# Performance work log

Hardware: AMD Instinct MI355X
Metric: run time of the kernel (lower is better)

Reference implementation:

```python
import jax, jax.numpy as jnp
import numpy as np

EMBED_DIM = 64
HEAD_NUM = 16
BS, QL, KL = 4, 2048, 2048


def setup_inputs() -> dict:
    key = jax.random.key(0)
    k1, k2, k3, k4, k5, k6, k7, k8 = jax.random.split(key, 8)
    d, H = EMBED_DIM, HEAD_NUM
    q_origin = jax.random.normal(k1, (BS, QL, d), dtype=jnp.float32)
    k_origin = jax.random.normal(k2, (BS, KL, d), dtype=jnp.float32)
    mask = jax.random.randint(k3, (BS, QL, KL), 0, 2).astype(bool)
    scale = 1.0 / np.sqrt(d)
    Wq = jax.random.normal(k4, (d, d * H), dtype=jnp.float32) * scale
    Wk = jax.random.normal(k5, (d, d * H), dtype=jnp.float32) * scale
    Wv = jax.random.normal(k6, (d, d * H), dtype=jnp.float32) * scale
    Wfc = jax.random.normal(k7, (d, d), dtype=jnp.float32) * scale
    bfc = jax.random.normal(k8, (d,), dtype=jnp.float32) * 0.01
    return {"q_origin": q_origin, "k_origin": k_origin, "mask": mask,
            "Wq": Wq, "Wk": Wk, "Wv": Wv, "Wfc": Wfc, "bfc": bfc}


def reference(q_origin, k_origin, mask, Wq, Wk, Wv, Wfc, bfc):
    bs, ql, d = q_origin.shape
    _, kl, _ = k_origin.shape
    H = Wq.shape[1] // d
    # projections, split into H heads of width d
    q = (q_origin @ Wq).reshape(bs, ql, H, d)   # bqhd
    k = (k_origin @ Wk).reshape(bs, kl, H, d)   # bkhd
    v = (k_origin @ Wv).reshape(bs, kl, H, d)   # bkhd
    scores = jnp.einsum('bqhd,bkhd->bhqk', q, k)
    scores = jnp.where(mask[:, None, :, :], -jnp.inf, scores)
    attn = jax.nn.softmax(scores / jnp.sqrt(jnp.asarray(d, scores.dtype)), axis=-1)
    attn = jnp.nan_to_num(attn)
    out = jnp.einsum('bhqk,bkhd->bqhd', attn, v)
    # torch code concatenates heads along the sequence axis: (bs, ql*H, d)
    out = out.reshape(bs, ql * H, d)
    return jnp.tanh(out @ Wfc + bfc)
```

## Files before the change

kernel.cpp:

```cpp
#include <hip/hip_runtime.h>
#include <hip/hip_bf16.h>

#define BSZ 4
#define SEQ 2048
#define NH  16
#define DH  64
#define TOK (BSZ*SEQ)
#define PROJC (NH*DH)

typedef __bf16 bf16x8 __attribute__((ext_vector_type(8)));
typedef float  f32x4  __attribute__((ext_vector_type(4)));
typedef float  f32x16 __attribute__((ext_vector_type(16)));
typedef unsigned int uint4v __attribute__((ext_vector_type(4)));
typedef unsigned int uint2v __attribute__((ext_vector_type(2)));

__device__ inline unsigned short f2bf(float f) {
    __bf16 h = (__bf16)f;
    return __builtin_bit_cast(unsigned short, h);
}

__device__ inline bf16x8 ld8(const unsigned short* p) {
    return __builtin_bit_cast(bf16x8, *reinterpret_cast<const uint4v*>(p));
}

__device__ inline float fexp2(float x) {
    float r;
    asm("v_exp_f32 %0, %1" : "=v"(r) : "v"(x));
    return r;
}

__device__ inline void gload16(const unsigned short* g, unsigned short* l) {
    __builtin_amdgcn_global_load_lds(
        (__attribute__((address_space(1))) void*)g,
        (__attribute__((address_space(3))) void*)l, 16, 0, 0);
}

__global__ __launch_bounds__(256) void prep_kernel(const float* __restrict__ q,
                                                   const float* __restrict__ k,
                                                   const float* __restrict__ Wq,
                                                   const float* __restrict__ Wk,
                                                   const float* __restrict__ Wv,
                                                   const float* __restrict__ Wfc,
                                                   unsigned short* __restrict__ qbf,
                                                   unsigned short* __restrict__ kbf,
                                                   unsigned short* __restrict__ WqT,
                                                   unsigned short* __restrict__ WkT,
                                                   unsigned short* __restrict__ WvT,
                                                   unsigned short* __restrict__ WfcT) {
    int bx = blockIdx.x;
    if (bx < 4096) {
        int idx = (bx & 2047) * 256 + threadIdx.x;
        if (bx < 2048) qbf[idx] = f2bf(q[idx]);
        else           kbf[idx] = f2bf(k[idx]);
        return;
    }
    bx -= 4096;
    const float* W; unsigned short* WT; int cols; int base;
    if      (bx < 256) { W = Wq;  WT = WqT;  cols = PROJC; base = bx; }
    else if (bx < 512) { W = Wk;  WT = WkT;  cols = PROJC; base = bx - 256; }
    else if (bx < 768) { W = Wv;  WT = WvT;  cols = PROJC; base = bx - 512; }
    else               { W = Wfc; WT = WfcT; cols = 64;    base = bx - 768; }
    int idx = base * 256 + threadIdx.x;
    int c = idx % cols, kk = idx / cols;
    WT[c * 64 + kk] = f2bf(W[kk * cols + c]);
}

__global__ __launch_bounds__(256) void maskpack_kernel(const int* __restrict__ mask,
                                                       unsigned long long* __restrict__ mbits) {
    size_t gid = (size_t)blockIdx.x * 256 + threadIdx.x;
    int lane = threadIdx.x & 63;
    unsigned long long bal = __ballot(mask[gid] != 0);
    if (lane == 0) mbits[gid >> 6] = bal;
}

__global__ __launch_bounds__(256) void proj_kernel(const unsigned short* __restrict__ qbf,
                                                   const unsigned short* __restrict__ kbf,
                                                   const unsigned short* __restrict__ WqT,
                                                   const unsigned short* __restrict__ WkT,
                                                   const unsigned short* __restrict__ WvT,
                                                   unsigned short* __restrict__ Qo,
                                                   unsigned short* __restrict__ Ko,
                                                   unsigned short* __restrict__ Vto) {
    __shared__ __align__(16) unsigned short TQ[64][72];
    __shared__ __align__(16) unsigned short TK[64][72];
    __shared__ __align__(16) unsigned short TV[64][72];
    int tid = threadIdx.x, w = tid >> 6, lane = tid & 63;
    int l15 = lane & 15, l4 = lane >> 4;
    int r0 = blockIdx.x * 64 + w * 16;
    int h = blockIdx.y;
    int c0 = h * 64;
    int b = blockIdx.x >> 5;
    size_t bh = (size_t)(b * NH + h);

    const unsigned short* aq = qbf + (r0 + l15) * 64 + l4 * 8;
    bf16x8 a0q = ld8(aq), a1q = ld8(aq + 32);
    const unsigned short* ak = kbf + (r0 + l15) * 64 + l4 * 8;
    bf16x8 a0k = ld8(ak), a1k = ld8(ak + 32);

    #pragma unroll
    for (int ct = 0; ct < 4; ++ct) {
        int wrow = (c0 + ct * 16 + l15) * 64 + l4 * 8;
        bf16x8 q0 = ld8(WqT + wrow), q1 = ld8(WqT + wrow + 32);
        bf16x8 k0 = ld8(WkT + wrow), k1 = ld8(WkT + wrow + 32);
        bf16x8 v0 = ld8(WvT + wrow), v1 = ld8(WvT + wrow + 32);
        f32x4 accq = {0.f,0.f,0.f,0.f}, acck = accq, accv = accq;
        accq = __builtin_amdgcn_mfma_f32_16x16x32_bf16(q0, a0q, accq, 0, 0, 0);
        accq = __builtin_amdgcn_mfma_f32_16x16x32_bf16(q1, a1q, accq, 0, 0, 0);
        acck = __builtin_amdgcn_mfma_f32_16x16x32_bf16(k0, a0k, acck, 0, 0, 0);
        acck = __builtin_amdgcn_mfma_f32_16x16x32_bf16(k1, a1k, acck, 0, 0, 0);
        accv = __builtin_amdgcn_mfma_f32_16x16x32_bf16(a0k, v0, accv, 0, 0, 0);
        accv = __builtin_amdgcn_mfma_f32_16x16x32_bf16(a1k, v1, accv, 0, 0, 0);
        uint2v pq, pk, pv;
        pq.x = (unsigned)f2bf(accq[0]) | ((unsigned)f2bf(accq[1]) << 16);
        pq.y = (unsigned)f2bf(accq[2]) | ((unsigned)f2bf(accq[3]) << 16);
        pk.x = (unsigned)f2bf(acck[0]) | ((unsigned)f2bf(acck[1]) << 16);
        pk.y = (unsigned)f2bf(acck[2]) | ((unsigned)f2bf(acck[3]) << 16);
        pv.x = (unsigned)f2bf(accv[0]) | ((unsigned)f2bf(accv[1]) << 16);
        pv.y = (unsigned)f2bf(accv[2]) | ((unsigned)f2bf(accv[3]) << 16);
        *reinterpret_cast<uint2v*>(&TQ[w * 16 + l15][ct * 16 + l4 * 4]) = pq;
        *reinterpret_cast<uint2v*>(&TK[w * 16 + l15][ct * 16 + l4 * 4]) = pk;
        *reinterpret_cast<uint2v*>(&TV[ct * 16 + l15][w * 16 + l4 * 4]) = pv;
    }
    __syncthreads();

    int rl8 = tid >> 3, chunk = tid & 7;
    int q0 = (blockIdx.x & 31) * 64;
    #pragma unroll
    for (int p = 0; p < 2; ++p) {
        int rl = p * 32 + rl8;
        uint4v vq = *reinterpret_cast<const uint4v*>(&TQ[rl][chunk * 8]);
        uint4v vk = *reinterpret_cast<const uint4v*>(&TK[rl][chunk * 8]);
        uint4v vv = *reinterpret_cast<const uint4v*>(&TV[rl][chunk * 8]);
        *reinterpret_cast<uint4v*>(Qo  + (bh * SEQ + q0 + rl) * 64 + chunk * 8) = vq;
        *reinterpret_cast<uint4v*>(Ko  + (bh * SEQ + q0 + rl) * 64 + chunk * 8) = vk;
        *reinterpret_cast<uint4v*>(Vto + (bh * 64 + rl) * SEQ + q0 + chunk * 8) = vv;
    }
}

__global__ __launch_bounds__(512, 4) void attn_kernel(const unsigned short* __restrict__ Q,
                                                      const unsigned short* __restrict__ K,
                                                      const unsigned short* __restrict__ Vt,
                                                      const unsigned long long* __restrict__ mbits,
                                                      unsigned short* __restrict__ O) {
    __shared__ __align__(16) unsigned short Ks[2][64 * 64];
    __shared__ __align__(16) unsigned short Vs[2][64 * 64];
    int tid = threadIdx.x, w = tid >> 6, lane = tid & 63;
    int l31 = lane & 31, hi = lane >> 5;
    int hi4 = hi * 4;

    int bid = blockIdx.x;
    int swz = (bid & 7) * 64 + (bid >> 3);
    int bh = swz >> 3;
    int qt = swz & 7;
    int b = bh >> 4;
    int qbase = qt * 256 + w * 32;

    const unsigned short* Qh = Q  + (size_t)bh * SEQ * 64;
    const unsigned short* Kh = K  + (size_t)bh * SEQ * 64;
    const unsigned short* Vh = Vt + (size_t)bh * 64 * SEQ;
    const unsigned long long* mrow =
        mbits + ((size_t)b * SEQ + qbase + l31) * (SEQ / 64);

    int row1 = (w << 3) + (lane >> 3);
    int sc1 = (lane & 7) ^ (row1 & 7);
    unsigned short* Kd0 = &Ks[0][0] + w * 512;
    unsigned short* Vd0 = &Vs[0][0] + w * 512;
    unsigned short* Kd1 = &Ks[1][0] + w * 512;
    unsigned short* Vd1 = &Vs[1][0] + w * 512;

    bf16x8 qf[4];
    #pragma unroll
    for (int s = 0; s < 4; ++s)
        qf[s] = ld8(Qh + (size_t)(qbase + l31) * 64 + s * 16 + hi * 8);

    bf16x8 ones;
    #pragma unroll
    for (int i = 0; i < 8; ++i) ones[i] = (__bf16)1.0f;

    f32x16 o0 = {0.f,0.f,0.f,0.f,0.f,0.f,0.f,0.f,0.f,0.f,0.f,0.f,0.f,0.f,0.f,0.f};
    f32x16 o1 = o0;
    f32x16 ellD = o0;
    const float C = 0.125f * 1.44269504088896f;

    auto stage_tile = [&](unsigned short* Kd, unsigned short* Vd, int nkb) {
        gload16(Kh + (size_t)(nkb + row1) * 64 + sc1 * 8, Kd);
        gload16(Vh + (size_t)row1 * SEQ + nkb + sc1 * 8, Vd);
    };

    auto compute_tile = [&](const unsigned short* Kc, const unsigned short* Vc, int kb) {
        unsigned long long wb = mrow[kb >> 6];
        #pragma unroll
        for (int kt = 0; kt < 2; ++kt) {
            f32x16 z = {0.f,0.f,0.f,0.f,0.f,0.f,0.f,0.f,0.f,0.f,0.f,0.f,0.f,0.f,0.f,0.f};
            int krow = kt * 32 + l31;
            #pragma unroll
            for (int s = 0; s < 4; ++s) {
                const unsigned short* kp =
                    Kc + krow * 64 + ((((s << 1) + hi) ^ (krow & 7)) << 3);
                z = __builtin_amdgcn_mfma_f32_32x32x16_bf16(ld8(kp), qf[s], z, 0, 0, 0);
            }
            unsigned wsh = (unsigned)(wb >> (kt * 32)) >> hi4;
            unsigned wpk[8];
            #pragma unroll
            for (int rq = 0; rq < 4; ++rq) {
                #pragma unroll
                for (int rr = 0; rr < 2; ++rr) {
                    float e[2];
                    #pragma unroll
                    for (int j = 0; j < 2; ++j) {
                        int pos = rq * 8 + 2 * rr + j;
                        int sx = (int)(wsh << (31 - pos)) >> 31;
                        float bias = __builtin_bit_cast(float, (unsigned)sx & 0xFF800000u);
                        e[j] = fexp2(__builtin_fmaf(z[rq * 4 + 2 * rr + j], C, bias));
                    }
                    wpk[rq * 2 + rr] = (unsigned)f2bf(e[0]) | ((unsigned)f2bf(e[1]) << 16);
                }
            }
            __builtin_amdgcn_s_setprio(1);
            #pragma unroll
            for (int sl = 0; sl < 2; ++sl) {
                uint4v aw = {wpk[sl * 4 + 0], wpk[sl * 4 + 1],
                             wpk[sl * 4 + 2], wpk[sl * 4 + 3]};
                bf16x8 af = __builtin_bit_cast(bf16x8, aw);
                ellD = __builtin_amdgcn_mfma_f32_32x32x16_bf16(af, ones, ellD, 0, 0, 0);
                int n = kt * 2 + sl;
                {
                    int vrow = l31;
                    int c0i = ((2 * n) ^ (vrow & 7)) << 3;
                    int c1i = ((2 * n + 1) ^ (vrow & 7)) << 3;
                    uint2v lo = *reinterpret_cast<const uint2v*>(Vc + vrow * 64 + c0i + hi4);
                    uint2v hh = *reinterpret_cast<const uint2v*>(Vc + vrow * 64 + c1i + hi4);
                    uint4v vw = {lo.x, lo.y, hh.x, hh.y};
                    o0 = __builtin_amdgcn_mfma_f32_32x32x16_bf16(
                        af, __builtin_bit_cast(bf16x8, vw), o0, 0, 0, 0);
                }
                {
                    int vrow = 32 + l31;
                    int c0i = ((2 * n) ^ (vrow & 7)) << 3;
                    int c1i = ((2 * n + 1) ^ (vrow & 7)) << 3;
                    uint2v lo = *reinterpret_cast<const uint2v*>(Vc + vrow * 64 + c0i + hi4);
                    uint2v hh = *reinterpret_cast<const uint2v*>(Vc + vrow * 64 + c1i + hi4);
                    uint4v vw = {lo.x, lo.y, hh.x, hh.y};
                    o1 = __builtin_amdgcn_mfma_f32_32x32x16_bf16(
                        af, __builtin_bit_cast(bf16x8, vw), o1, 0, 0, 0);
                }
            }
            __builtin_amdgcn_s_setprio(0);
        }
    };

    stage_tile(Kd0, Vd0, 0);
    __syncthreads();

    for (int kb = 0; kb < SEQ; kb += 128) {
        stage_tile(Kd1, Vd1, kb + 64);
        compute_tile(&Ks[0][0], &Vs[0][0], kb);
        __syncthreads();
        if (kb + 128 < SEQ) stage_tile(Kd0, Vd0, kb + 128);
        compute_tile(&Ks[1][0], &Vs[1][0], kb + 64);
        __syncthreads();
    }
    #pragma unroll
    for (int reg = 0; reg < 16; ++reg) {
        float l = ellD[reg];
        float rcp = (l == 0.f) ? 0.f : __builtin_amdgcn_rcpf(l);
        int ql = (reg & 3) + 8 * (reg >> 2) + hi4;
        size_t base = ((size_t)bh * SEQ + qbase + ql) * 64 + l31;
        O[base]      = f2bf(o0[reg] * rcp);
        O[base + 32] = f2bf(o1[reg] * rcp);
    }
}

__global__ __launch_bounds__(256) void fc_kernel(const unsigned short* __restrict__ O,
                                                 const unsigned short* __restrict__ WfcT,
                                                 const float* __restrict__ bfc,
                                                 float* __restrict__ out) {
    int tid = threadIdx.x, w = tid >> 6, lane = tid & 63;
    int l15 = lane & 15, l4 = lane >> 4;
    int r0 = blockIdx.x * 64 + w * 16;

    int row = r0 + l15;
    int h = row & 15, t_ = row >> 4;
    int q = t_ & 2047, b = t_ >> 11;
    const unsigned short* op = O + (((size_t)(b * NH + h)) * SEQ + q) * 64 + l4 * 8;
    bf16x8 a0 = ld8(op), a1 = ld8(op + 32);

    for (int ct = 0; ct < 4; ++ct) {
        const unsigned short* wp = WfcT + (ct * 16 + l15) * 64 + l4 * 8;
        bf16x8 b0 = ld8(wp), b1 = ld8(wp + 32);
        f32x4 acc = {0.f, 0.f, 0.f, 0.f};
        acc = __builtin_amdgcn_mfma_f32_16x16x32_bf16(b0, a0, acc, 0, 0, 0);
        acc = __builtin_amdgcn_mfma_f32_16x16x32_bf16(b1, a1, acc, 0, 0, 0);
        f32x4 bv = *reinterpret_cast<const f32x4*>(bfc + ct * 16 + l4 * 4);
        f32x4 st;
        #pragma unroll
        for (int r = 0; r < 4; ++r) {
            float x = acc[r] + bv[r];
            x = fminf(fmaxf(x, -9.f), 9.f);
            float t = fexp2(x * 2.88539008177793f);
            st[r] = (t - 1.f) * __builtin_amdgcn_rcpf(t + 1.f);
        }
        *reinterpret_cast<f32x4*>(out + (size_t)row * 64 + ct * 16 + l4 * 4) = st;
    }
}

extern "C" void kernel_launch(void* const* d_in, const int* in_sizes, int n_in,
                              void* d_out, int out_size, void* d_ws, size_t ws_size,
                              hipStream_t stream) {
    const float* q_origin = (const float*)d_in[0];
    const float* k_origin = (const float*)d_in[1];
    const int*   mask     = (const int*)d_in[2];
    const float* Wq       = (const float*)d_in[3];
    const float* Wk       = (const float*)d_in[4];
    const float* Wv       = (const float*)d_in[5];
    const float* Wfc      = (const float*)d_in[6];
    const float* bfc      = (const float*)d_in[7];
    float* out = (float*)d_out;

    unsigned short* ws = (unsigned short*)d_ws;
    unsigned short* qbf  = ws;
    unsigned short* kbf  = qbf  + TOK * DH;
    unsigned short* WqT  = kbf  + TOK * DH;
    unsigned short* WkT  = WqT  + 64 * PROJC;
    unsigned short* WvT  = WkT  + 64 * PROJC;
    unsigned short* WfcT = WvT  + 64 * PROJC;
    unsigned short* Qb   = WfcT + 64 * 64;
    unsigned short* Kb   = Qb   + (size_t)BSZ * NH * SEQ * DH;
    unsigned short* Vtb  = Kb   + (size_t)BSZ * NH * SEQ * DH;
    unsigned short* Ob   = Vtb  + (size_t)BSZ * NH * SEQ * DH;
    unsigned long long* mbits = (unsigned long long*)d_ws;

    prep_kernel<<<4880, 256, 0, stream>>>(q_origin, k_origin, Wq, Wk, Wv, Wfc,
                                          qbf, kbf, WqT, WkT, WvT, WfcT);
    proj_kernel<<<dim3(TOK / 64, NH), 256, 0, stream>>>(
        qbf, kbf, WqT, WkT, WvT, Qb, Kb, Vtb);
    maskpack_kernel<<<(size_t)BSZ * SEQ * SEQ / 256, 256, 0, stream>>>(mask, mbits);
    attn_kernel<<<512, 512, 0, stream>>>(Qb, Kb, Vtb, mbits, Ob);
    fc_kernel<<<(size_t)BSZ * SEQ * NH / 64, 256, 0, stream>>>(Ob, WfcT, bfc, out);
}
```

Before: 175.0 us.

## Fuse output FC projection and tanh into attention kernel epilogue

The attention kernel now stages its normalized per-wave output tile into the freed K/V shared memory with an XOR swizzle. It then runs the 64x64 FC projection with 32x32x16 MFMAs, adds the bias and applies tanh before writing fp32 results directly. This removes the separate fc_kernel launch and the bf16 O round-trip through global memory. In exchange the attention epilogue gets longer and needs more registers, and WfcT is reloaded from global by every wave.

```diff
diff --git a/kernel.cpp b/kernel.cpp
--- a/kernel.cpp
+++ b/kernel.cpp
@@ -141,7 +141,9 @@
                                                       const unsigned short* __restrict__ K,
                                                       const unsigned short* __restrict__ Vt,
                                                       const unsigned long long* __restrict__ mbits,
-                                                      unsigned short* __restrict__ O) {
+                                                      const unsigned short* __restrict__ WfcT,
+                                                      const float* __restrict__ bfc,
+                                                      float* __restrict__ out) {
     __shared__ __align__(16) unsigned short Ks[2][64 * 64];
     __shared__ __align__(16) unsigned short Vs[2][64 * 64];
     int tid = threadIdx.x, w = tid >> 6, lane = tid & 63;
@@ -260,47 +262,49 @@
         compute_tile(&Ks[1][0], &Vs[1][0], kb + 64);
         __syncthreads();
     }
+
+    unsigned short* Ot = ((w < 4) ? &Ks[0][0] : &Vs[0][0]) + (w & 3) * 2048;
+
     #pragma unroll
     for (int reg = 0; reg < 16; ++reg) {
         float l = ellD[reg];
         float rcp = (l == 0.f) ? 0.f : __builtin_amdgcn_rcpf(l);
         int ql = (reg & 3) + 8 * (reg >> 2) + hi4;
-        size_t base = ((size_t)bh * SEQ + qbase + ql) * 64 + l31;
-        O[base]      = f2bf(o0[reg] * rcp);
-        O[base + 32] = f2bf(o1[reg] * rcp);
-    }
-}
-
-__global__ __launch_bounds__(256) void fc_kernel(const unsigned short* __restrict__ O,
-                                                 const unsigned short* __restrict__ WfcT,
-                                                 const float* __restrict__ bfc,
-                                                 float* __restrict__ out) {
-    int tid = threadIdx.x, w = tid >> 6, lane = tid & 63;
-    int l15 = lane & 15, l4 = lane >> 4;
-    int r0 = blockIdx.x * 64 + w * 16;
-
-    int row = r0 + l15;
-    int h = row & 15, t_ = row >> 4;
-    int q = t_ & 2047, b = t_ >> 11;
-    const unsigned short* op = O + (((size_t)(b * NH + h)) * SEQ + q) * 64 + l4 * 8;
-    bf16x8 a0 = ld8(op), a1 = ld8(op + 32);
-
-    for (int ct = 0; ct < 4; ++ct) {
-        const unsigned short* wp = WfcT + (ct * 16 + l15) * 64 + l4 * 8;
-        bf16x8 b0 = ld8(wp), b1 = ld8(wp + 32);
-        f32x4 acc = {0.f, 0.f, 0.f, 0.f};
-        acc = __builtin_amdgcn_mfma_f32_16x16x32_bf16(b0, a0, acc, 0, 0, 0);
-        acc = __builtin_amdgcn_mfma_f32_16x16x32_bf16(b1, a1, acc, 0, 0, 0);
-        f32x4 bv = *reinterpret_cast<const f32x4*>(bfc + ct * 16 + l4 * 4);
-        f32x4 st;
+        int ch0 = (l31 >> 3) ^ (ql & 7);
+        int ch1 = ((l31 >> 3) + 4) ^ (ql & 7);
+        Ot[ql * 64 + ch0 * 8 + (l31 & 7)] = f2bf(o0[reg] * rcp);
+        Ot[ql * 64 + ch1 * 8 + (l31 & 7)] = f2bf(o1[reg] * rcp);
+    }
+    bf16x8 of[4];
+    #pragma unroll
+    for (int s = 0; s < 4; ++s) {
+        int cs = (s * 2 + hi) ^ (l31 & 7);
+        of[s] = ld8(Ot + l31 * 64 + cs * 8);
+    }
+    int qrow = qbase + l31;
+    size_t orow = ((size_t)b * SEQ + qrow) * NH + (bh & 15);
+    #pragma unroll
+    for (int ctile = 0; ctile < 2; ++ctile) {
+        f32x16 acc = {0.f,0.f,0.f,0.f,0.f,0.f,0.f,0.f,0.f,0.f,0.f,0.f,0.f,0.f,0.f,0.f};
         #pragma unroll
-        for (int r = 0; r < 4; ++r) {
-            float x = acc[r] + bv[r];
-            x = fminf(fmaxf(x, -9.f), 9.f);
-            float t = fexp2(x * 2.88539008177793f);
-            st[r] = (t - 1.f) * __builtin_amdgcn_rcpf(t + 1.f);
+        for (int s = 0; s < 4; ++s) {
+            bf16x8 wf = ld8(WfcT + (ctile * 32 + l31) * 64 + s * 16 + hi * 8);
+            acc = __builtin_amdgcn_mfma_f32_32x32x16_bf16(wf, of[s], acc, 0, 0, 0);
         }
-        *reinterpret_cast<f32x4*>(out + (size_t)row * 64 + ct * 16 + l4 * 4) = st;
+        #pragma unroll
+        for (int g = 0; g < 4; ++g) {
+            int cbase = ctile * 32 + 8 * g + hi4;
+            f32x4 bv = *reinterpret_cast<const f32x4*>(bfc + cbase);
+            f32x4 st;
+            #pragma unroll
+            for (int r = 0; r < 4; ++r) {
+                float x = acc[g * 4 + r] + bv[r];
+                x = fminf(fmaxf(x, -9.f), 9.f);
+                float t = fexp2(x * 2.88539008177793f);
+                st[r] = (t - 1.f) * __builtin_amdgcn_rcpf(t + 1.f);
+            }
+            *reinterpret_cast<f32x4*>(out + orow * 64 + cbase) = st;
+        }
     }
 }
 
@@ -327,7 +331,6 @@
     unsigned short* Qb   = WfcT + 64 * 64;
     unsigned short* Kb   = Qb   + (size_t)BSZ * NH * SEQ * DH;
     unsigned short* Vtb  = Kb   + (size_t)BSZ * NH * SEQ * DH;
-    unsigned short* Ob   = Vtb  + (size_t)BSZ * NH * SEQ * DH;
     unsigned long long* mbits = (unsigned long long*)d_ws;
 
     prep_kernel<<<4880, 256, 0, stream>>>(q_origin, k_origin, Wq, Wk, Wv, Wfc,
@@ -335,6 +338,5 @@
     proj_kernel<<<dim3(TOK / 64, NH), 256, 0, stream>>>(
         qbf, kbf, WqT, WkT, WvT, Qb, Kb, Vtb);
     maskpack_kernel<<<(size_t)BSZ * SEQ * SEQ / 256, 256, 0, stream>>>(mask, mbits);
-    attn_kernel<<<512, 512, 0, stream>>>(Qb, Kb, Vtb, mbits, Ob);
-    fc_kernel<<<(size_t)BSZ * SEQ * NH / 64, 256, 0, stream>>>(Ob, WfcT, bfc, out);
-}
+    attn_kernel<<<512, 512, 0, stream>>>(Qb, Kb, Vtb, mbits, WfcT, bfc, out);
+}
```

New measurement: 166.3 us. 1.05x faster.
